# Optimization experiments

Hardware: AMD Instinct MI355X
Metric: run time of the kernel (lower is better)

The kernel has to match this reference:

```python
import jax, jax.numpy as jnp
import numpy as np

# ---- Haar DWT (levels=1, mode='zero'), matches pytorch_wavelets ordering ----
# For even H,W and filter length 2, zero-pad haar analysis reduces to
# non-overlapping 2x2 blocks. Subband order after the two 1D analyses
# (width first, then height): LL, (w-lo,h-hi), (w-hi,h-lo), HH.

def haar_dwt(x):
    a = x[..., 0::2, 0::2]
    b = x[..., 0::2, 1::2]
    c = x[..., 1::2, 0::2]
    d = x[..., 1::2, 1::2]
    ll = (a + b + c + d) * 0.5
    h0 = (a + b - c - d) * 0.5   # lo-width, hi-height
    h1 = (a - b + c - d) * 0.5   # hi-width, lo-height
    hh = (a - b - c + d) * 0.5
    return ll, jnp.stack([h0, h1, hh], axis=2)  # yh: (b,c,3,h/2,w/2)


def _interleave(u, v, axis):
    # interleave two equal-shaped arrays along `axis` (negative axis)
    s = list(u.shape)
    s[axis] *= 2
    return jnp.stack([u, v], axis=axis + len(u.shape) + 1).reshape(s)


def haar_idwt(ll, yh):
    h0, h1, hh = yh[:, :, 0], yh[:, :, 1], yh[:, :, 2]
    a = (ll + h0 + h1 + hh) * 0.5
    b = (ll + h0 - h1 - hh) * 0.5
    c = (ll - h0 + h1 - hh) * 0.5
    d = (ll - h0 - h1 + hh) * 0.5
    top = _interleave(a, b, -1)   # even rows
    bot = _interleave(c, d, -1)   # odd rows
    return _interleave(top, bot, -2)


def batched_dynamic_conv(feat, kernels, pad):
    """feat: (b,cin,h,w), kernels: (b,cout,cin,kh,kw) -> (b,cout,h,w).
    Per-sample kernels via grouped conv (batch as groups)."""
    bsz, cin, h, w = feat.shape
    cout, kh, kw = kernels.shape[1], kernels.shape[3], kernels.shape[4]
    lhs = feat.reshape(1, bsz * cin, h, w)
    rhs = kernels.reshape(bsz * cout, cin, kh, kw)
    out = jax.lax.conv_general_dilated(
        lhs, rhs, window_strides=(1, 1), padding=[(pad, pad), (pad, pad)],
        dimension_numbers=('NCHW', 'OIHW', 'NCHW'), feature_group_count=bsz)
    return out.reshape(bsz, cout, h, w)


def _dyn_conv_subband(feat, sub_kernels, attn_w, attn_b, pad=1):
    # attention: 1x1 conv -> global avg pool -> softmax over kernel_num
    logits = jnp.einsum('bchw,kc->bk', feat, attn_w) / (feat.shape[-2] * feat.shape[-1]) + attn_b
    att = jax.nn.softmax(logits, axis=1)                       # (b,K)
    kernels = jnp.einsum('bk,koiuv->boiuv', att, sub_kernels)  # (b,cout,cin,kh,kw)
    return batched_dynamic_conv(feat, kernels, pad)


def setup_inputs() -> dict:
    key = jax.random.key(0)
    k1, k2, k3, k4 = jax.random.split(key, 4)
    B, C, H, W = 8, 64, 128, 128
    K, SUB, COUT, KS = 4, 4, 64, 3  # kernel_num, 1+3*levels, out_channels, kernel_size
    return {
        'x': jax.random.normal(k1, (B, C, H, W), dtype=jnp.float32),
        'wt_kernels': jax.random.normal(k2, (K, SUB, COUT, C, KS, KS), dtype=jnp.float32) * 0.02,
        'attn_w': jax.random.normal(k3, (K, C), dtype=jnp.float32) * 0.1,
        'attn_b': jnp.zeros((K,), dtype=jnp.float32),
    }


def reference(x, wt_kernels, attn_w, attn_b):
    ll, yh = haar_dwt(x)
    subbands = [ll, yh[:, :, 0], yh[:, :, 1], yh[:, :, 2]]
    outs = [_dyn_conv_subband(sb, wt_kernels[:, i], attn_w, attn_b, pad=1)
            for i, sb in enumerate(subbands)]
    rec_yh = jnp.stack(outs[1:4], axis=2)  # (b,cout,3,h/2,w/2)
    return haar_idwt(outs[0], rec_yh)
```

## Files before the change

kernel.cpp:

```cpp
#include <hip/hip_runtime.h>
#include <hip/hip_bf16.h>
#include <math.h>


typedef __bf16 bf16x8 __attribute__((ext_vector_type(8)));
typedef float f32x4 __attribute__((ext_vector_type(4)));

__device__ __forceinline__ bf16x8 as_bf16x8(uint4 u) {
    union { uint4 a; bf16x8 b; } c; c.a = u; return c.b;
}
__device__ __forceinline__ unsigned short bf16bits(float f) {
    __hip_bfloat16 h = __float2bfloat16(f);
    union { __hip_bfloat16 h; unsigned short u; } c; c.h = h; return c.u;
}

__global__ __launch_bounds__(256)
void dwt_kernel(const float* __restrict__ x, unsigned short* __restrict__ feats,
                float* __restrict__ sums) {
    __shared__ uint4 sT[2304];
    unsigned short* sTu = (unsigned short*)sT;
    int y = blockIdx.x, b = blockIdx.y;
    int t = threadIdx.x;
    int c = t >> 2, q = t & 3;

    const float4* r0 = (const float4*)x + ((size_t)(b * 64 + c) * 128 + 2 * y) * 32 + q * 8;
    const float4* r1 = r0 + 32;

    float s0 = 0.f, s1 = 0.f, s2 = 0.f, s3 = 0.f;
    #pragma unroll
    for (int i = 0; i < 8; ++i) {
        float4 p = r0[i], qq = r1[i];
        int xo = q * 16 + 2 * i;
        {
            float a = p.x, bb = p.y, cc = qq.x, dd = qq.y;
            float ll = (a + bb + cc + dd) * 0.5f, h0 = (a + bb - cc - dd) * 0.5f;
            float h1 = (a - bb + cc - dd) * 0.5f, hh = (a - bb - cc + dd) * 0.5f;
            s0 += ll; s1 += h0; s2 += h1; s3 += hh;
            sTu[0 * 4608 + xo * 72 + c] = bf16bits(ll);
            sTu[1 * 4608 + xo * 72 + c] = bf16bits(h0);
            sTu[2 * 4608 + xo * 72 + c] = bf16bits(h1);
            sTu[3 * 4608 + xo * 72 + c] = bf16bits(hh);
        }
        {
            float a = p.z, bb = p.w, cc = qq.z, dd = qq.w;
            float ll = (a + bb + cc + dd) * 0.5f, h0 = (a + bb - cc - dd) * 0.5f;
            float h1 = (a - bb + cc - dd) * 0.5f, hh = (a - bb - cc + dd) * 0.5f;
            s0 += ll; s1 += h0; s2 += h1; s3 += hh;
            sTu[0 * 4608 + (xo + 1) * 72 + c] = bf16bits(ll);
            sTu[1 * 4608 + (xo + 1) * 72 + c] = bf16bits(h0);
            sTu[2 * 4608 + (xo + 1) * 72 + c] = bf16bits(h1);
            sTu[3 * 4608 + (xo + 1) * 72 + c] = bf16bits(hh);
        }
    }
    s0 += __shfl_xor(s0, 1); s0 += __shfl_xor(s0, 2);
    s1 += __shfl_xor(s1, 1); s1 += __shfl_xor(s1, 2);
    s2 += __shfl_xor(s2, 1); s2 += __shfl_xor(s2, 2);
    s3 += __shfl_xor(s3, 1); s3 += __shfl_xor(s3, 2);
    if (q == 0) {
        float* sp = sums + (size_t)(b * 64 + c) * 4;
        atomicAdd(sp + 0, s0); atomicAdd(sp + 1, s1);
        atomicAdd(sp + 2, s2); atomicAdd(sp + 3, s3);
    }
    __syncthreads();
    uint4* fch = (uint4*)feats;
    for (int e = t; e < 2048; e += 256) {
        int s = e >> 9, xx = (e >> 3) & 63, ck = e & 7;
        fch[(size_t)((b * 4 + s) * 64 + y) * 512 + xx * 8 + ck] = sT[s * 576 + xx * 9 + ck];
    }
}

__global__ __launch_bounds__(128)
void attn_kernel(const float* __restrict__ sums, const float* __restrict__ attn_w,
                 const float* __restrict__ attn_b, float* __restrict__ att) {
    int t = threadIdx.x;
    int b = t >> 4, sub = (t >> 2) & 3, k = t & 3;
    float acc = 0.f;
    for (int c = 0; c < 64; ++c)
        acc += attn_w[k * 64 + c] * sums[((size_t)b * 64 + c) * 4 + sub];
    float logit = acc * (1.0f / 4096.0f) + attn_b[k];
    float m = logit;
    m = fmaxf(m, __shfl_xor(m, 1));
    m = fmaxf(m, __shfl_xor(m, 2));
    float e = expf(logit - m);
    float s = e;
    s += __shfl_xor(s, 1);
    s += __shfl_xor(s, 2);
    att[t] = e / s;
}

__global__ __launch_bounds__(256)
void mix_kernel(const float* __restrict__ wt, const float* __restrict__ att,
                unsigned short* __restrict__ wmix) {
    int tap = blockIdx.y, bz = blockIdx.z;
    int sub = bz & 3;
    int flat2 = blockIdx.x * 512 + threadIdx.x * 2;
    int co = flat2 >> 6, ci = flat2 & 63;
    const float* a4 = att + (size_t)bz * 4;
    const size_t ks = 147456;
    size_t base = (((size_t)sub * 64 + co) * 64 + ci) * 9 + tap;
    float v0 = a4[0] * wt[base] + a4[1] * wt[base + ks]
             + a4[2] * wt[base + 2 * ks] + a4[3] * wt[base + 3 * ks];
    float v1 = a4[0] * wt[base + 9] + a4[1] * wt[base + ks + 9]
             + a4[2] * wt[base + 2 * ks + 9] + a4[3] * wt[base + 3 * ks + 9];
    ushort2 o; o.x = bf16bits(v0); o.y = bf16bits(v1);
    *(ushort2*)(wmix + (size_t)bz * 36864 + tap * 4096 + flat2) = o;
}

__global__ __launch_bounds__(256, 2)
void conv_kernel(const unsigned short* __restrict__ feats,
                 const unsigned short* __restrict__ wmix,
                 unsigned short* __restrict__ conv_out) {
    __shared__ uint4 sA[1296];
    __shared__ uint4 sW[2304];
    int tile = blockIdx.x, sub = blockIdx.y, b = blockIdx.z;
    int y0 = (tile >> 2) * 16, x0 = (tile & 3) * 16;
    int t = threadIdx.x, w = t >> 6, l = t & 63;
    int l16 = l & 15, kg = l >> 4;
    const uint4* fch = (const uint4*)feats + (size_t)(b * 4 + sub) * 32768;
    const uint4* wch = (const uint4*)wmix + (size_t)(b * 4 + sub) * 4608;

    f32x4 acc[4][4];
    #pragma unroll
    for (int r = 0; r < 4; ++r)
        #pragma unroll
        for (int nn = 0; nn < 4; ++nn)
            acc[r][nn] = (f32x4){0.f, 0.f, 0.f, 0.f};

    #pragma unroll
    for (int ck8 = 0; ck8 < 8; ck8 += 4) {
        __syncthreads();
        for (int e = t; e < 1296; e += 256) {
            int py = e / 72, rr = e - py * 72, px = rr >> 2, g = rr & 3;
            int gy = y0 - 1 + py, gx = x0 - 1 + px;
            uint4 v = make_uint4(0u, 0u, 0u, 0u);
            if ((unsigned)gy < 64u && (unsigned)gx < 64u)
                v = fch[(gy * 64 + gx) * 8 + ck8 + g];
            sA[e] = v;
        }
        for (int e = t; e < 2304; e += 256) {
            int tap = e >> 8, co = (e >> 2) & 63, g = e & 3;
            sW[e] = wch[tap * 512 + co * 8 + ck8 + g];
        }
        __syncthreads();
        #pragma unroll
        for (int tap = 0; tap < 9; ++tap) {
            int dy = tap / 3, dx = tap - dy * 3;
            bf16x8 bfr[4];
            #pragma unroll
            for (int nn = 0; nn < 4; ++nn)
                bfr[nn] = as_bf16x8(sW[tap * 256 + (nn * 16 + l16) * 4 + kg]);
            #pragma unroll
            for (int r = 0; r < 4; ++r) {
                bf16x8 af = as_bf16x8(sA[((w * 4 + r + dy) * 18 + l16 + dx) * 4 + kg]);
                #pragma unroll
                for (int nn = 0; nn < 4; ++nn)
                    acc[r][nn] = __builtin_amdgcn_mfma_f32_16x16x32_bf16(
                        af, bfr[nn], acc[r][nn], 0, 0, 0);
            }
        }
    }
    size_t obase = (size_t)(b * 4 + sub) * 262144;
    #pragma unroll
    for (int r = 0; r < 4; ++r) {
        int yy = y0 + w * 4 + r;
        #pragma unroll
        for (int nn = 0; nn < 4; ++nn) {
            int co = nn * 16 + l16;
            #pragma unroll
            for (int j = 0; j < 4; ++j) {
                int xx = x0 + kg * 4 + j;
                conv_out[obase + ((size_t)yy * 64 + xx) * 64 + co] = bf16bits(acc[r][nn][j]);
            }
        }
    }
}

__global__ __launch_bounds__(256)
void idwt_kernel(const unsigned short* __restrict__ conv_out,
                 float* __restrict__ out) {
    __shared__ uint4 sT[2304];
    int y = blockIdx.x, b = blockIdx.y;
    int t = threadIdx.x;
    const uint4* cch = (const uint4*)conv_out;
    for (int e = t; e < 2048; e += 256) {
        int s = e >> 9, xx = (e >> 3) & 63, ck = e & 7;
        sT[s * 576 + xx * 9 + ck] = cch[(size_t)(b * 4 + s) * 32768 + y * 512 + xx * 8 + ck];
    }
    __syncthreads();
    int xx = t & 63, cw = t >> 6;
    #pragma unroll
    for (int half = 0; half < 2; ++half) {
        int ckk = half * 4 + cw;
        bf16x8 v0 = as_bf16x8(sT[0 * 576 + xx * 9 + ckk]);
        bf16x8 v1 = as_bf16x8(sT[1 * 576 + xx * 9 + ckk]);
        bf16x8 v2 = as_bf16x8(sT[2 * 576 + xx * 9 + ckk]);
        bf16x8 v3 = as_bf16x8(sT[3 * 576 + xx * 9 + ckk]);
        #pragma unroll
        for (int j = 0; j < 8; ++j) {
            int c = ckk * 8 + j;
            float ll = (float)v0[j], h0 = (float)v1[j];
            float h1 = (float)v2[j], hh = (float)v3[j];
            float a = (ll + h0 + h1 + hh) * 0.5f;
            float bb = (ll + h0 - h1 - hh) * 0.5f;
            float cc = (ll - h0 + h1 - hh) * 0.5f;
            float dd = (ll - h0 - h1 + hh) * 0.5f;
            float2* o0 = (float2*)out + ((size_t)(b * 64 + c) * 128 + 2 * y) * 64 + xx;
            o0[0]  = make_float2(a, bb);
            o0[64] = make_float2(cc, dd);
        }
    }
}

extern "C" void kernel_launch(void* const* d_in, const int* in_sizes, int n_in,
                              void* d_out, int out_size, void* d_ws, size_t ws_size,
                              hipStream_t stream) {
    const float* x  = (const float*)d_in[0];
    const float* wt = (const float*)d_in[1];
    const float* aw = (const float*)d_in[2];
    const float* ab = (const float*)d_in[3];
    float* out = (float*)d_out;
    char* ws = (char*)d_ws;

    float* sums              = (float*)ws;
    float* att               = (float*)(ws + 8192);
    unsigned short* feats    = (unsigned short*)(ws + 8704);
    unsigned short* wmix     = (unsigned short*)(ws + 8704 + 16777216);
    unsigned short* conv_out = (unsigned short*)(ws + 8704 + 16777216 + 2359296);

    hipMemsetAsync(sums, 0, 8192, stream);
    hipLaunchKernelGGL(dwt_kernel, dim3(64, 8), dim3(256), 0, stream, x, feats, sums);
    hipLaunchKernelGGL(attn_kernel, dim3(1), dim3(128), 0, stream, sums, aw, ab, att);
    hipLaunchKernelGGL(mix_kernel, dim3(8, 9, 32), dim3(256), 0, stream, wt, att, wmix);
    hipLaunchKernelGGL(conv_kernel, dim3(16, 4, 8), dim3(256), 0, stream, feats, wmix, conv_out);
    hipLaunchKernelGGL(idwt_kernel, dim3(64, 8), dim3(256), 0, stream, conv_out, out);
}
```

Baseline: 140.4 us.

## Fuse attention softmax into weight-mix kernel and coalesce DWT input loads

```diff
diff --git a/kernel.cpp b/kernel.cpp
--- a/kernel.cpp
+++ b/kernel.cpp
@@ -23,14 +23,15 @@
     int t = threadIdx.x;
     int c = t >> 2, q = t & 3;
 
-    const float4* r0 = (const float4*)x + ((size_t)(b * 64 + c) * 128 + 2 * y) * 32 + q * 8;
+    const float4* r0 = (const float4*)x + ((size_t)(b * 64 + c) * 128 + 2 * y) * 32;
     const float4* r1 = r0 + 32;
 
     float s0 = 0.f, s1 = 0.f, s2 = 0.f, s3 = 0.f;
     #pragma unroll
     for (int i = 0; i < 8; ++i) {
-        float4 p = r0[i], qq = r1[i];
-        int xo = q * 16 + 2 * i;
+        int f = i * 4 + q;
+        float4 p = r0[f], qq = r1[f];
+        int xo = 2 * f;
         {
             float a = p.x, bb = p.y, cc = qq.x, dd = qq.y;
             float ll = (a + bb + cc + dd) * 0.5f, h0 = (a + bb - cc - dd) * 0.5f;
@@ -69,41 +70,45 @@
     }
 }
 
-__global__ __launch_bounds__(128)
-void attn_kernel(const float* __restrict__ sums, const float* __restrict__ attn_w,
-                 const float* __restrict__ attn_b, float* __restrict__ att) {
+__global__ __launch_bounds__(256)
+void mix_kernel(const float* __restrict__ wt, const float* __restrict__ attn_w,
+                const float* __restrict__ attn_b, const float* __restrict__ sums,
+                unsigned short* __restrict__ wmix) {
+    __shared__ float sLw[4][576];
+    __shared__ float satt[8][4];
+    int co = blockIdx.x, sub = blockIdx.y;
     int t = threadIdx.x;
-    int b = t >> 4, sub = (t >> 2) & 3, k = t & 3;
-    float acc = 0.f;
-    for (int c = 0; c < 64; ++c)
-        acc += attn_w[k * 64 + c] * sums[((size_t)b * 64 + c) * 4 + sub];
-    float logit = acc * (1.0f / 4096.0f) + attn_b[k];
-    float m = logit;
-    m = fmaxf(m, __shfl_xor(m, 1));
-    m = fmaxf(m, __shfl_xor(m, 2));
-    float e = expf(logit - m);
-    float s = e;
-    s += __shfl_xor(s, 1);
-    s += __shfl_xor(s, 2);
-    att[t] = e / s;
-}
-
-__global__ __launch_bounds__(256)
-void mix_kernel(const float* __restrict__ wt, const float* __restrict__ att,
-                unsigned short* __restrict__ wmix) {
-    int tap = blockIdx.y, bz = blockIdx.z;
-    int sub = bz & 3;
-    int flat2 = blockIdx.x * 512 + threadIdx.x * 2;
-    int co = flat2 >> 6, ci = flat2 & 63;
-    const float* a4 = att + (size_t)bz * 4;
-    const size_t ks = 147456;
-    size_t base = (((size_t)sub * 64 + co) * 64 + ci) * 9 + tap;
-    float v0 = a4[0] * wt[base] + a4[1] * wt[base + ks]
-             + a4[2] * wt[base + 2 * ks] + a4[3] * wt[base + 3 * ks];
-    float v1 = a4[0] * wt[base + 9] + a4[1] * wt[base + ks + 9]
-             + a4[2] * wt[base + 2 * ks + 9] + a4[3] * wt[base + 3 * ks + 9];
-    ushort2 o; o.x = bf16bits(v0); o.y = bf16bits(v1);
-    *(ushort2*)(wmix + (size_t)bz * 36864 + tap * 4096 + flat2) = o;
+
+    if (t < 32) {
+        int b = t >> 2, k = t & 3;
+        float acc = 0.f;
+        #pragma unroll 8
+        for (int c = 0; c < 64; ++c)
+            acc += attn_w[k * 64 + c] * sums[((size_t)(b * 64 + c) << 2) + sub];
+        float logit = acc * (1.0f / 4096.0f) + attn_b[k];
+        float m = fmaxf(logit, __shfl_xor(logit, 1));
+        m = fmaxf(m, __shfl_xor(m, 2));
+        float e = expf(logit - m);
+        float s = e + __shfl_xor(e, 1);
+        s += __shfl_xor(s, 2);
+        satt[b][k] = e / s;
+    }
+    for (int e = t; e < 2304; e += 256) {
+        int k = e / 576, r = e - k * 576;
+        sLw[k][r] = wt[((size_t)(k * 4 + sub) * 64 + co) * 576 + r];
+    }
+    __syncthreads();
+    #pragma unroll
+    for (int j = 0; j < 18; ++j) {
+        int idx = j * 256 + t;
+        int b = idx / 576;
+        int r = idx - b * 576;
+        int tap = r >> 6, ci = r & 63;
+        int wi = ci * 9 + tap;
+        float v = satt[b][0] * sLw[0][wi] + satt[b][1] * sLw[1][wi]
+                + satt[b][2] * sLw[2][wi] + satt[b][3] * sLw[3][wi];
+        wmix[((size_t)(b * 4 + sub) * 9 + tap) * 4096 + co * 64 + ci] = bf16bits(v);
+    }
 }
 
 __global__ __launch_bounds__(256, 2)
@@ -222,15 +227,13 @@
     char* ws = (char*)d_ws;
 
     float* sums              = (float*)ws;
-    float* att               = (float*)(ws + 8192);
-    unsigned short* feats    = (unsigned short*)(ws + 8704);
-    unsigned short* wmix     = (unsigned short*)(ws + 8704 + 16777216);
-    unsigned short* conv_out = (unsigned short*)(ws + 8704 + 16777216 + 2359296);
+    unsigned short* feats    = (unsigned short*)(ws + 8192);
+    unsigned short* wmix     = (unsigned short*)(ws + 8192 + 16777216);
+    unsigned short* conv_out = (unsigned short*)(ws + 8192 + 16777216 + 2359296);
 
     hipMemsetAsync(sums, 0, 8192, stream);
     hipLaunchKernelGGL(dwt_kernel, dim3(64, 8), dim3(256), 0, stream, x, feats, sums);
-    hipLaunchKernelGGL(attn_kernel, dim3(1), dim3(128), 0, stream, sums, aw, ab, att);
-    hipLaunchKernelGGL(mix_kernel, dim3(8, 9, 32), dim3(256), 0, stream, wt, att, wmix);
+    hipLaunchKernelGGL(mix_kernel, dim3(64, 4), dim3(256), 0, stream, wt, aw, ab, sums, wmix);
     hipLaunchKernelGGL(conv_kernel, dim3(16, 4, 8), dim3(256), 0, stream, feats, wmix, conv_out);
     hipLaunchKernelGGL(idwt_kernel, dim3(64, 8), dim3(256), 0, stream, conv_out, out);
 }
```

After: 134.4 us. -4.3%, faster.
